# Kernel optimization log

Hardware: AMD Instinct MI355X
Metric: run time of the kernel (lower is better)

Reference implementation:

```python
import jax, jax.numpy as jnp
import numpy as np

DECAY = 0.99
EPS = 1e-05


def setup_inputs() -> dict:
    key = jax.random.key(0)
    k1, k2, k3 = jax.random.split(key, 3)
    B, H, W, D, K = 16, 32, 32, 256, 8192
    x = jax.random.normal(k1, (B, H, W, D), dtype=jnp.float32)
    embed = jax.random.normal(k2, (D, K), dtype=jnp.float32)
    cluster_size = jnp.zeros((K,), dtype=jnp.float32)
    embed_avg = jax.random.normal(k3, (D, K), dtype=jnp.float32)
    return {"x": x, "embed": embed, "cluster_size": cluster_size, "embed_avg": embed_avg}


def reference(x, embed, cluster_size, embed_avg):
    D, K = embed.shape
    flat = x.reshape(-1, D)  # (N, D)
    # squared L2 distances: ||f||^2 - 2 f.e + ||e||^2  -> (N, K)
    dist = (flat * flat).sum(1, keepdims=True) - 2.0 * (flat @ embed) + (embed * embed).sum(0, keepdims=True)
    idx = jnp.argmin(dist, axis=1)  # (N,)
    quantize = jnp.take(embed.T, idx, axis=0).reshape(x.shape)  # (B,H,W,D)
    # EMA codebook statistics (training branch)
    onehot_sum = jnp.zeros((K,), dtype=flat.dtype).at[idx].add(1.0)  # (K,)
    embed_sum = jax.ops.segment_sum(flat, idx, num_segments=K).T  # (D, K)
    new_cluster_size = cluster_size * DECAY + (1.0 - DECAY) * onehot_sum
    new_embed_avg = embed_avg * DECAY + (1.0 - DECAY) * embed_sum
    n = new_cluster_size.sum()
    cs = (new_cluster_size + EPS) / (n + K * EPS) * n
    new_embed = new_embed_avg / cs[None, :]
    latent_loss = jnp.mean((jax.lax.stop_gradient(quantize) - x) ** 2)
    quantize_st = x + jax.lax.stop_gradient(quantize - x)  # straight-through
    return quantize_st, latent_loss, new_embed, new_cluster_size, new_embed_avg
```

## Files before the change

kernel.cpp:

```cpp
#include <hip/hip_runtime.h>

constexpr int NROWS = 16384;
constexpr int D     = 256;
constexpr int K     = 8192;

constexpr float DECAY = 0.99f;
constexpr float OMD   = 0.01f;
constexpr float EPSF  = 1e-5f;

constexpr size_t OUT_Q    = 0;
constexpr size_t OUT_LOSS = (size_t)NROWS * D;
constexpr size_t OUT_NE   = OUT_LOSS + 1;
constexpr size_t OUT_NCS  = OUT_NE + (size_t)D * K;
constexpr size_t OUT_NEA  = OUT_NCS + K;

constexpr size_t WS_KEYS  = 0;
constexpr size_t WS_ENORM = WS_KEYS + (size_t)NROWS * 8;
constexpr size_t WS_XH    = ((WS_ENORM + (size_t)K * 4 + 4095) / 4096) * 4096;
constexpr size_t WS_XL    = WS_XH + (size_t)NROWS * D * 2;
constexpr size_t WS_EHT   = WS_XL + (size_t)NROWS * D * 2;
constexpr size_t WS_ELT   = WS_EHT + (size_t)K * D * 2;

typedef unsigned int u32;
typedef unsigned short u16;
typedef unsigned long long u64;
typedef __attribute__((ext_vector_type(8))) short bf16x8;
typedef __attribute__((ext_vector_type(4))) float f32x4;
typedef __attribute__((ext_vector_type(4))) u32 u32x4;
typedef __attribute__((ext_vector_type(2))) u32 u32x2;

__device__ __forceinline__ u16 f2bf(float f) {
    u32 u = __float_as_uint(f);
    u32 r = (u + 0x7FFFu + ((u >> 16) & 1u)) >> 16;
    return (u16)r;
}
__device__ __forceinline__ float bf2f(u16 h) {
    return __uint_as_float((u32)h << 16);
}

__device__ __forceinline__ void gl_lds16(const void* g, void* l) {
    __builtin_amdgcn_global_load_lds(
        (const __attribute__((address_space(1))) u32*)g,
        (__attribute__((address_space(3))) u32*)l, 16, 0, 0);
}

__global__ void pre_kernel(const float* __restrict__ x,
                           const float* __restrict__ embed,
                           const float* __restrict__ cluster_size,
                           u16* __restrict__ xh, u16* __restrict__ xl,
                           u16* __restrict__ ehT, u16* __restrict__ elT,
                           float* __restrict__ enorm,
                           u64* __restrict__ keys,
                           float* __restrict__ ncs_out,
                           float* __restrict__ loss_out) {
    const int bid = blockIdx.x;
    const int t   = threadIdx.x;

    if (bid >= 176) {
        size_t g = (size_t)(bid - 176) * 256 + t;
        float4 v = *(const float4*)&x[g * 4];
        u16 h0 = f2bf(v.x), h1 = f2bf(v.y), h2 = f2bf(v.z), h3 = f2bf(v.w);
        u16 l0 = f2bf(v.x - bf2f(h0)), l1 = f2bf(v.y - bf2f(h1));
        u16 l2 = f2bf(v.z - bf2f(h2)), l3 = f2bf(v.w - bf2f(h3));
        u32x2 hp, lp;
        hp.x = (u32)h0 | ((u32)h1 << 16); hp.y = (u32)h2 | ((u32)h3 << 16);
        lp.x = (u32)l0 | ((u32)l1 << 16); lp.y = (u32)l2 | ((u32)l3 << 16);
        ((u32x2*)xh)[g] = hp;
        ((u32x2*)xl)[g] = lp;
        return;
    }
    if (bid >= 144) {
        int i = (bid - 144) * 256 + t;
        ncs_out[i] = DECAY * cluster_size[i];
        return;
    }
    if (bid >= 128) {
        int idx = (bid - 128) * 256 + t;
        #pragma unroll
        for (int j = 0; j < 4; ++j) keys[j * 4096 + idx] = ~0ull;
        if (bid == 128 && t == 0) loss_out[0] = 0.f;
        return;
    }

    __shared__ float tile[64][68];
    const int kBase = bid * 64;
    const int dl = t >> 2;
    const int kl = t >> 2;
    const int qq = t & 3;
    float nacc = 0.f;

    for (int dBase = 0; dBase < D; dBase += 64) {
        #pragma unroll
        for (int i = 0; i < 4; ++i) {
            int kk = qq * 16 + i * 4;
            float4 v = *(const float4*)&embed[(size_t)(dBase + dl) * K + kBase + kk];
            tile[dl][kk + 0] = v.x; tile[dl][kk + 1] = v.y;
            tile[dl][kk + 2] = v.z; tile[dl][kk + 3] = v.w;
        }
        __syncthreads();
        u32 hp[8], lp[8];
        float s = 0.f;
        #pragma unroll
        for (int j = 0; j < 16; ++j) {
            float f = tile[qq * 16 + j][kl];
            s = fmaf(f, f, s);
            u16 hb = f2bf(f);
            u16 lb = f2bf(f - bf2f(hb));
            if (j & 1) { hp[j >> 1] |= (u32)hb << 16; lp[j >> 1] |= (u32)lb << 16; }
            else       { hp[j >> 1]  = hb;            lp[j >> 1]  = lb; }
        }
        s += __shfl_down(s, 1);
        s += __shfl_down(s, 2);
        if (qq == 0) nacc += s;

        size_t o = ((size_t)(kBase + kl) * D + dBase + qq * 16) >> 1;
        u32x4 a, b;
        a.x = hp[0]; a.y = hp[1]; a.z = hp[2]; a.w = hp[3];
        b.x = hp[4]; b.y = hp[5]; b.z = hp[6]; b.w = hp[7];
        *(u32x4*)&((u32*)ehT)[o]     = a;
        *(u32x4*)&((u32*)ehT)[o + 4] = b;
        a.x = lp[0]; a.y = lp[1]; a.z = lp[2]; a.w = lp[3];
        b.x = lp[4]; b.y = lp[5]; b.z = lp[6]; b.w = lp[7];
        *(u32x4*)&((u32*)elT)[o]     = a;
        *(u32x4*)&((u32*)elT)[o + 4] = b;
        __syncthreads();
    }
    if (qq == 0) enorm[kBase + kl] = nacc;
}

__global__ __launch_bounds__(512, 2) void dist_argmin_mfma(
        const u16* __restrict__ xh, const u16* __restrict__ xl,
        const u16* __restrict__ ehT, const u16* __restrict__ elT,
        const float* __restrict__ enorm,
        u64* __restrict__ keys) {
    __shared__ u16 lds[2][32768];

    const int tid  = threadIdx.x;
    const int lane = tid & 63;
    const int wave = tid >> 6;
    const int wm   = wave >> 1;
    const int wn   = wave & 1;
    const int r = lane & 15, g = lane >> 4;
    const int rowBase = blockIdx.y * 256;
    const int colBase = blockIdx.x * 256;

    f32x4 acc[4][8];
    #pragma unroll
    for (int i = 0; i < 4; ++i)
        #pragma unroll
        for (int j = 0; j < 8; ++j) acc[i][j] = (f32x4)0.f;

    const int chunk8 = (((tid & 3) ^ ((tid >> 3) & 3)) * 8);
    const int arow   = tid >> 2;
    const size_t a0 = (size_t)(rowBase + arow) * D + chunk8;
    const size_t a1 = (size_t)(rowBase + 128 + arow) * D + chunk8;
    const int bmat   = tid >> 8;
    const int qrow   = (tid & 255) >> 2;
    const int bcol0  = (qrow < 32) ? qrow : (96 + qrow);
    const size_t bq0 = (size_t)(colBase + bcol0) * D + chunk8;
    const u16* bsrc  = bmat ? elT : ehT;

    const int kx = (g ^ ((r >> 1) & 3)) * 8;

    #define ST_XH0(buf, ks) gl_lds16(&xh[a0 + (ks) * 32], &lds[buf][tid * 8])
    #define ST_XH1(buf, ks) gl_lds16(&xh[a1 + (ks) * 32], &lds[buf][4096 + tid * 8])
    #define ST_XL0(buf, ks) gl_lds16(&xl[a0 + (ks) * 32], &lds[buf][8192 + tid * 8])
    #define ST_XL1(buf, ks) gl_lds16(&xl[a1 + (ks) * 32], &lds[buf][12288 + tid * 8])
    #define ST_B(buf, ks, q) \
        gl_lds16(&bsrc[bq0 + (size_t)(q) * 32 * D + (ks) * 32], \
                 &lds[buf][16384 + (q) * 4096 + tid * 8])

    ST_B(0, 0, 0); ST_XH0(0, 0); ST_B(0, 0, 1); ST_XH1(0, 0);
    ST_B(0, 0, 2); ST_XL0(0, 0); ST_B(0, 0, 3); ST_XL1(0, 0);
    ST_B(1, 1, 0); ST_XH0(1, 1); ST_B(1, 1, 1); ST_XH1(1, 1);
    ST_B(1, 1, 2); ST_XL0(1, 1);

    bf16x8 fah[4], fal[4];
    bf16x8 fbhA[2], fblA[2], fbhB[2], fblB[2];

    #define RD_A(Lp)                                                              \
        do { _Pragma("unroll") for (int i_ = 0; i_ < 4; ++i_) {                   \
            fah[i_] = *(const bf16x8*)&(Lp)[((wm * 64 + i_ * 16 + r) * 32) + kx]; \
            fal[i_] = *(const bf16x8*)&(Lp)[8192 + ((wm * 64 + i_ * 16 + r) * 32) + kx]; \
        } } while (0)

    #define RD_B(Lp, p, FH, FL)                                                   \
        do { _Pragma("unroll") for (int jj_ = 0; jj_ < 2; ++jj_) {                \
            const int qr_ = wn * 32 + jj_ * 16 + r;                               \
            (FH)[jj_] = *(const bf16x8*)&(Lp)[16384 + (p) * 4096 + qr_ * 32 + kx];        \
            (FL)[jj_] = *(const bf16x8*)&(Lp)[16384 + (p) * 4096 + 2048 + qr_ * 32 + kx]; \
        } } while (0)

    #define MFMA_PH(p, FH, FL)                                                    \
        do { _Pragma("unroll") for (int i_ = 0; i_ < 4; ++i_) {                   \
            acc[i_][2*(p)]   = __builtin_amdgcn_mfma_f32_16x16x32_bf16(fah[i_], (FH)[0], acc[i_][2*(p)],   0, 0, 0); \
            acc[i_][2*(p)]   = __builtin_amdgcn_mfma_f32_16x16x32_bf16(fah[i_], (FL)[0], acc[i_][2*(p)],   0, 0, 0); \
            acc[i_][2*(p)]   = __builtin_amdgcn_mfma_f32_16x16x32_bf16(fal[i_], (FH)[0], acc[i_][2*(p)],   0, 0, 0); \
            acc[i_][2*(p)+1] = __builtin_amdgcn_mfma_f32_16x16x32_bf16(fah[i_], (FH)[1], acc[i_][2*(p)+1], 0, 0, 0); \
            acc[i_][2*(p)+1] = __builtin_amdgcn_mfma_f32_16x16x32_bf16(fah[i_], (FL)[1], acc[i_][2*(p)+1], 0, 0, 0); \
            acc[i_][2*(p)+1] = __builtin_amdgcn_mfma_f32_16x16x32_bf16(fal[i_], (FH)[1], acc[i_][2*(p)+1], 0, 0, 0); \
        } } while (0)

    #define LGKM4() asm volatile("s_waitcnt lgkmcnt(4)" ::: "memory"); \
                    __builtin_amdgcn_sched_barrier(0)
    #define LGKM0() asm volatile("s_waitcnt lgkmcnt(0)" ::: "memory"); \
                    __builtin_amdgcn_sched_barrier(0)

    #pragma unroll
    for (int ks = 0; ks < 8; ++ks) {
        const int c = ks & 1;
        const u16* L = lds[c];

        if (ks == 7) asm volatile("s_waitcnt vmcnt(0)" ::: "memory");
        else         asm volatile("s_waitcnt vmcnt(6)" ::: "memory");
        __builtin_amdgcn_s_barrier();
        __builtin_amdgcn_sched_barrier(0);

        RD_A(L);
        RD_B(L, 0, fbhA, fblA);
        RD_B(L, 1, fbhB, fblB);
        if (ks <= 6) { ST_B(c ^ 1, ks + 1, 3); ST_XL1(c ^ 1, ks + 1); }
        LGKM4();
        __builtin_amdgcn_s_setprio(1);
        MFMA_PH(0, fbhA, fblA);
        __builtin_amdgcn_s_setprio(0);
        __builtin_amdgcn_s_barrier();
        __builtin_amdgcn_sched_barrier(0);

        RD_B(L, 2, fbhA, fblA);
        if (ks <= 5) { ST_B(c, ks + 2, 0); ST_XH0(c, ks + 2); }
        LGKM4();
        __builtin_amdgcn_s_setprio(1);
        MFMA_PH(1, fbhB, fblB);
        __builtin_amdgcn_s_setprio(0);
        __builtin_amdgcn_s_barrier();
        __builtin_amdgcn_sched_barrier(0);

        RD_B(L, 3, fbhB, fblB);
        if (ks <= 5) { ST_B(c, ks + 2, 1); ST_XH1(c, ks + 2); }
        LGKM4();
        __builtin_amdgcn_s_setprio(1);
        MFMA_PH(2, fbhA, fblA);
        __builtin_amdgcn_s_setprio(0);
        __builtin_amdgcn_s_barrier();
        __builtin_amdgcn_sched_barrier(0);

        if (ks <= 5) { ST_B(c, ks + 2, 2); ST_XL0(c, ks + 2); }
        LGKM0();
        __builtin_amdgcn_s_setprio(1);
        MFMA_PH(3, fbhB, fblB);
        __builtin_amdgcn_s_setprio(0);
        __builtin_amdgcn_s_barrier();
        __builtin_amdgcn_sched_barrier(0);
    }
    #undef MFMA_PH
    #undef RD_A
    #undef RD_B
    #undef LGKM4
    #undef LGKM0
    #undef ST_XH0
    #undef ST_XH1
    #undef ST_XL0
    #undef ST_XL1
    #undef ST_B

    float en[8];
    #pragma unroll
    for (int j = 0; j < 8; ++j) en[j] = enorm[colBase + wn * 128 + j * 16 + r];

    #pragma unroll
    for (int i = 0; i < 4; ++i) {
        #pragma unroll
        for (int p4 = 0; p4 < 4; ++p4) {
            float best = __builtin_inff();
            int bk = 0;
            #pragma unroll
            for (int j = 0; j < 8; ++j) {
                float s = fmaf(-2.f, acc[i][j][p4], en[j]);
                int ccol = colBase + wn * 128 + j * 16 + r;
                if (s < best) { best = s; bk = ccol; }
            }
            u32 u = __float_as_uint(best);
            u ^= (u >> 31) ? 0xFFFFFFFFu : 0x80000000u;
            u64 key = ((u64)u << 32) | (u32)bk;
            #pragma unroll
            for (int m = 1; m < 16; m <<= 1) {
                u64 o = __shfl_xor(key, m);
                key = o < key ? o : key;
            }
            if (r == 0)
                atomicMin(&keys[rowBase + wm * 64 + i * 16 + g * 4 + p4], key);
        }
    }
}

__global__ void postprocess_kernel(const float* __restrict__ x,
                                   const u16* __restrict__ ehT,
                                   const u16* __restrict__ elT,
                                   const u64* __restrict__ keys,
                                   float* __restrict__ q_out,
                                   float* __restrict__ loss_out,
                                   float* __restrict__ acc_t,
                                   float* __restrict__ ncs_out) {
    const int w    = threadIdx.x >> 6;
    const int lane = threadIdx.x & 63;
    const int r    = blockIdx.x * 4 + w;
    const u32 k = (u32)keys[r];

    float4 xv = *(const float4*)&x[(size_t)r * D + lane * 4];
    size_t uo = ((size_t)k * D >> 1) + lane * 2;
    u32x2 hp = *(const u32x2*)&((const u32*)ehT)[uo];
    u32x2 lp = *(const u32x2*)&((const u32*)elT)[uo];
    float q0 = __uint_as_float(hp.x << 16)         + __uint_as_float(lp.x << 16);
    float q1 = __uint_as_float(hp.x & 0xFFFF0000u) + __uint_as_float(lp.x & 0xFFFF0000u);
    float q2 = __uint_as_float(hp.y << 16)         + __uint_as_float(lp.y << 16);
    float q3 = __uint_as_float(hp.y & 0xFFFF0000u) + __uint_as_float(lp.y & 0xFFFF0000u);
    *(float4*)&q_out[(size_t)r * D + lane * 4] = make_float4(q0, q1, q2, q3);

    float* dst = &acc_t[(size_t)k * D + lane * 4];
    atomicAdd(dst + 0, xv.x);
    atomicAdd(dst + 1, xv.y);
    atomicAdd(dst + 2, xv.z);
    atomicAdd(dst + 3, xv.w);
    if (lane == 0) atomicAdd(&ncs_out[k], OMD);

    float d0 = q0 - xv.x, d1 = q1 - xv.y, d2 = q2 - xv.z, d3 = q3 - xv.w;
    float lsum = fmaf(d0, d0, fmaf(d1, d1, fmaf(d2, d2, d3 * d3)));
    #pragma unroll
    for (int off = 32; off > 0; off >>= 1) lsum += __shfl_down(lsum, off);
    __shared__ float wsum[4];
    if (lane == 0) wsum[w] = lsum;
    __syncthreads();
    if (threadIdx.x == 0) {
        float s = wsum[0] + wsum[1] + wsum[2] + wsum[3];
        atomicAdd(loss_out, s * (1.0f / ((float)NROWS * (float)D)));
    }
}

__global__ void ema_finalize_kernel(const float* __restrict__ embed_avg,
                                    const float* __restrict__ acc_t,
                                    const float* __restrict__ ncs_out,
                                    const float* __restrict__ cluster_size,
                                    float* __restrict__ nea_out,
                                    float* __restrict__ ne_out) {
    __shared__ float tile[64][68];
    __shared__ float wsums[4];
    const int kBase = blockIdx.x * 64;
    const int dBase = blockIdx.y * 64;
    const int t = threadIdx.x;

    float cs_part = 0.f;
    #pragma unroll
    for (int j = 0; j < K / 256; ++j) cs_part += cluster_size[j * 256 + t];
    #pragma unroll
    for (int off = 32; off > 0; off >>= 1) cs_part += __shfl_down(cs_part, off);
    if ((t & 63) == 0) wsums[t >> 6] = cs_part;

    {
        const int kl = t >> 2, q = t & 3;
        #pragma unroll
        for (int i = 0; i < 4; ++i) {
            int dd = q * 16 + i * 4;
            float4 v = *(const float4*)&acc_t[(size_t)(kBase + kl) * D + dBase + dd];
            tile[kl][dd + 0] = v.x; tile[kl][dd + 1] = v.y;
            tile[kl][dd + 2] = v.z; tile[kl][dd + 3] = v.w;
        }
    }
    __syncthreads();
    const float cssum = wsums[0] + wsums[1] + wsums[2] + wsums[3];
    const float n = DECAY * cssum + OMD * (float)NROWS;
    const float inv_na = 1.0f / (n + (float)K * EPSF);
    const int dl = t >> 2, q = t & 3;
    #pragma unroll
    for (int i = 0; i < 4; ++i) {
        int kk = q * 16 + i * 4;
        size_t o = (size_t)(dBase + dl) * K + kBase + kk;
        float4 ea = *(const float4*)&embed_avg[o];
        float4 nea, ne;
        #pragma unroll
        for (int c = 0; c < 4; ++c) {
            float v  = DECAY * ((const float*)&ea)[c] + OMD * tile[kk + c][dl];
            float cs = (ncs_out[kBase + kk + c] + EPSF) * inv_na * n;
            ((float*)&nea)[c] = v;
            ((float*)&ne)[c]  = v / cs;
        }
        *(float4*)&nea_out[o] = nea;
        *(float4*)&ne_out[o]  = ne;
    }
}

extern "C" void kernel_launch(void* const* d_in, const int* in_sizes, int n_in,
                              void* d_out, int out_size, void* d_ws, size_t ws_size,
                              hipStream_t stream) {
    (void)in_sizes; (void)n_in; (void)out_size; (void)ws_size;
    const float* x            = (const float*)d_in[0];
    const float* embed        = (const float*)d_in[1];
    const float* cluster_size = (const float*)d_in[2];
    const float* embed_avg    = (const float*)d_in[3];
    float* out = (float*)d_out;

    char* ws = (char*)d_ws;
    u64*   keys  = (u64*)(ws + WS_KEYS);
    float* enorm = (float*)(ws + WS_ENORM);
    u16*   xh    = (u16*)(ws + WS_XH);
    u16*   xl    = (u16*)(ws + WS_XL);
    u16*   ehT   = (u16*)(ws + WS_EHT);
    u16*   elT   = (u16*)(ws + WS_ELT);
    float* acc_t = (float*)(ws + WS_XH);

    float* q_out    = out + OUT_Q;
    float* loss_out = out + OUT_LOSS;
    float* ne_out   = out + OUT_NE;
    float* ncs_out  = out + OUT_NCS;
    float* nea_out  = out + OUT_NEA;

    pre_kernel<<<dim3(176 + NROWS * D / 4 / 256), dim3(256), 0, stream>>>(
        x, embed, cluster_size, xh, xl, ehT, elT, enorm, keys, ncs_out, loss_out);

    dist_argmin_mfma<<<dim3(K / 256, NROWS / 256), dim3(512), 0, stream>>>(
        xh, xl, ehT, elT, enorm, keys);

    hipMemsetAsync(acc_t, 0, (size_t)K * D * 4, stream);
    postprocess_kernel<<<dim3(NROWS / 4), dim3(256), 0, stream>>>(
        x, ehT, elT, keys, q_out, loss_out, acc_t, ncs_out);
    ema_finalize_kernel<<<dim3(K / 64, D / 64), dim3(256), 0, stream>>>(
        embed_avg, acc_t, ncs_out, cluster_size, nea_out, ne_out);
}
```

Measured before the change: 298.5 us.

## Split codebook conversion blocks and precompute cluster-size sum once

```diff
diff --git a/kernel.cpp b/kernel.cpp
--- a/kernel.cpp
+++ b/kernel.cpp
@@ -16,7 +16,8 @@
 
 constexpr size_t WS_KEYS  = 0;
 constexpr size_t WS_ENORM = WS_KEYS + (size_t)NROWS * 8;
-constexpr size_t WS_XH    = ((WS_ENORM + (size_t)K * 4 + 4095) / 4096) * 4096;
+constexpr size_t WS_NSUM  = WS_ENORM + (size_t)K * 4;
+constexpr size_t WS_XH    = ((WS_NSUM + 4096) / 4096) * 4096;
 constexpr size_t WS_XL    = WS_XH + (size_t)NROWS * D * 2;
 constexpr size_t WS_EHT   = WS_XL + (size_t)NROWS * D * 2;
 constexpr size_t WS_ELT   = WS_EHT + (size_t)K * D * 2;
@@ -52,12 +53,13 @@
                            float* __restrict__ enorm,
                            u64* __restrict__ keys,
                            float* __restrict__ ncs_out,
-                           float* __restrict__ loss_out) {
+                           float* __restrict__ loss_out,
+                           float* __restrict__ nsum) {
     const int bid = blockIdx.x;
     const int t   = threadIdx.x;
 
-    if (bid >= 176) {
-        size_t g = (size_t)(bid - 176) * 256 + t;
+    if (bid >= 593) {
+        size_t g = (size_t)(bid - 593) * 256 + t;
         float4 v = *(const float4*)&x[g * 4];
         u16 h0 = f2bf(v.x), h1 = f2bf(v.y), h2 = f2bf(v.z), h3 = f2bf(v.w);
         u16 l0 = f2bf(v.x - bf2f(h0)), l1 = f2bf(v.y - bf2f(h1));
@@ -69,63 +71,81 @@
         ((u32x2*)xl)[g] = lp;
         return;
     }
-    if (bid >= 144) {
-        int i = (bid - 144) * 256 + t;
+    if (bid == 592) {
+        __shared__ float ws4[4];
+        float v = 0.f;
+        #pragma unroll
+        for (int j = 0; j < K / 256; ++j) v += cluster_size[j * 256 + t];
+        #pragma unroll
+        for (int off = 32; off > 0; off >>= 1) v += __shfl_down(v, off);
+        if ((t & 63) == 0) ws4[t >> 6] = v;
+        __syncthreads();
+        if (t == 0) {
+            nsum[0] = ws4[0] + ws4[1] + ws4[2] + ws4[3];
+            loss_out[0] = 0.f;
+        }
+        return;
+    }
+    if (bid >= 560) {
+        int i = (bid - 560) * 256 + t;
         ncs_out[i] = DECAY * cluster_size[i];
         return;
     }
-    if (bid >= 128) {
-        int idx = (bid - 128) * 256 + t;
+    if (bid >= 544) {
+        int idx = (bid - 544) * 256 + t;
         #pragma unroll
         for (int j = 0; j < 4; ++j) keys[j * 4096 + idx] = ~0ull;
-        if (bid == 128 && t == 0) loss_out[0] = 0.f;
         return;
     }
+    if (bid >= 512) {
+        int k = (bid - 512) * 256 + t;
+        float a0 = 0.f, a1 = 0.f, a2 = 0.f, a3 = 0.f;
+        for (int d = 0; d < D; d += 4) {
+            float e0 = embed[(size_t)(d + 0) * K + k];
+            float e1 = embed[(size_t)(d + 1) * K + k];
+            float e2 = embed[(size_t)(d + 2) * K + k];
+            float e3 = embed[(size_t)(d + 3) * K + k];
+            a0 = fmaf(e0, e0, a0); a1 = fmaf(e1, e1, a1);
+            a2 = fmaf(e2, e2, a2); a3 = fmaf(e3, e3, a3);
+        }
+        enorm[k] = (a0 + a1) + (a2 + a3);
+        return;
+    }
 
     __shared__ float tile[64][68];
-    const int kBase = bid * 64;
-    const int dl = t >> 2;
-    const int kl = t >> 2;
-    const int qq = t & 3;
-    float nacc = 0.f;
-
-    for (int dBase = 0; dBase < D; dBase += 64) {
+    const int kBase = (bid >> 2) * 64;
+    const int dBase = (bid & 3) * 64;
+    {
+        const int dl = t >> 2, q = t & 3;
         #pragma unroll
         for (int i = 0; i < 4; ++i) {
-            int kk = qq * 16 + i * 4;
+            int kk = q * 16 + i * 4;
             float4 v = *(const float4*)&embed[(size_t)(dBase + dl) * K + kBase + kk];
             tile[dl][kk + 0] = v.x; tile[dl][kk + 1] = v.y;
             tile[dl][kk + 2] = v.z; tile[dl][kk + 3] = v.w;
         }
-        __syncthreads();
-        u32 hp[8], lp[8];
-        float s = 0.f;
-        #pragma unroll
-        for (int j = 0; j < 16; ++j) {
-            float f = tile[qq * 16 + j][kl];
-            s = fmaf(f, f, s);
-            u16 hb = f2bf(f);
-            u16 lb = f2bf(f - bf2f(hb));
-            if (j & 1) { hp[j >> 1] |= (u32)hb << 16; lp[j >> 1] |= (u32)lb << 16; }
-            else       { hp[j >> 1]  = hb;            lp[j >> 1]  = lb; }
-        }
-        s += __shfl_down(s, 1);
-        s += __shfl_down(s, 2);
-        if (qq == 0) nacc += s;
-
-        size_t o = ((size_t)(kBase + kl) * D + dBase + qq * 16) >> 1;
-        u32x4 a, b;
-        a.x = hp[0]; a.y = hp[1]; a.z = hp[2]; a.w = hp[3];
-        b.x = hp[4]; b.y = hp[5]; b.z = hp[6]; b.w = hp[7];
-        *(u32x4*)&((u32*)ehT)[o]     = a;
-        *(u32x4*)&((u32*)ehT)[o + 4] = b;
-        a.x = lp[0]; a.y = lp[1]; a.z = lp[2]; a.w = lp[3];
-        b.x = lp[4]; b.y = lp[5]; b.z = lp[6]; b.w = lp[7];
-        *(u32x4*)&((u32*)elT)[o]     = a;
-        *(u32x4*)&((u32*)elT)[o + 4] = b;
-        __syncthreads();
-    }
-    if (qq == 0) enorm[kBase + kl] = nacc;
+    }
+    __syncthreads();
+    const int kl = t >> 2, q = t & 3;
+    u32 hp[8], lp[8];
+    #pragma unroll
+    for (int j = 0; j < 16; ++j) {
+        float f = tile[q * 16 + j][kl];
+        u16 hb = f2bf(f);
+        u16 lb = f2bf(f - bf2f(hb));
+        if (j & 1) { hp[j >> 1] |= (u32)hb << 16; lp[j >> 1] |= (u32)lb << 16; }
+        else       { hp[j >> 1]  = hb;            lp[j >> 1]  = lb; }
+    }
+    size_t o = ((size_t)(kBase + kl) * D + dBase + q * 16) >> 1;
+    u32x4 a, b;
+    a.x = hp[0]; a.y = hp[1]; a.z = hp[2]; a.w = hp[3];
+    b.x = hp[4]; b.y = hp[5]; b.z = hp[6]; b.w = hp[7];
+    *(u32x4*)&((u32*)ehT)[o]     = a;
+    *(u32x4*)&((u32*)ehT)[o + 4] = b;
+    a.x = lp[0]; a.y = lp[1]; a.z = lp[2]; a.w = lp[3];
+    b.x = lp[4]; b.y = lp[5]; b.z = lp[6]; b.w = lp[7];
+    *(u32x4*)&((u32*)elT)[o]     = a;
+    *(u32x4*)&((u32*)elT)[o + 4] = b;
 }
 
 __global__ __launch_bounds__(512, 2) void dist_argmin_mfma(
@@ -340,22 +360,13 @@
 __global__ void ema_finalize_kernel(const float* __restrict__ embed_avg,
                                     const float* __restrict__ acc_t,
                                     const float* __restrict__ ncs_out,
-                                    const float* __restrict__ cluster_size,
+                                    const float* __restrict__ nsum,
                                     float* __restrict__ nea_out,
                                     float* __restrict__ ne_out) {
     __shared__ float tile[64][68];
-    __shared__ float wsums[4];
     const int kBase = blockIdx.x * 64;
     const int dBase = blockIdx.y * 64;
     const int t = threadIdx.x;
-
-    float cs_part = 0.f;
-    #pragma unroll
-    for (int j = 0; j < K / 256; ++j) cs_part += cluster_size[j * 256 + t];
-    #pragma unroll
-    for (int off = 32; off > 0; off >>= 1) cs_part += __shfl_down(cs_part, off);
-    if ((t & 63) == 0) wsums[t >> 6] = cs_part;
-
     {
         const int kl = t >> 2, q = t & 3;
         #pragma unroll
@@ -367,8 +378,7 @@
         }
     }
     __syncthreads();
-    const float cssum = wsums[0] + wsums[1] + wsums[2] + wsums[3];
-    const float n = DECAY * cssum + OMD * (float)NROWS;
+    const float n = DECAY * nsum[0] + OMD * (float)NROWS;
     const float inv_na = 1.0f / (n + (float)K * EPSF);
     const int dl = t >> 2, q = t & 3;
     #pragma unroll
@@ -402,6 +412,7 @@
     char* ws = (char*)d_ws;
     u64*   keys  = (u64*)(ws + WS_KEYS);
     float* enorm = (float*)(ws + WS_ENORM);
+    float* nsum  = (float*)(ws + WS_NSUM);
     u16*   xh    = (u16*)(ws + WS_XH);
     u16*   xl    = (u16*)(ws + WS_XL);
     u16*   ehT   = (u16*)(ws + WS_EHT);
@@ -414,8 +425,9 @@
     float* ncs_out  = out + OUT_NCS;
     float* nea_out  = out + OUT_NEA;
 
-    pre_kernel<<<dim3(176 + NROWS * D / 4 / 256), dim3(256), 0, stream>>>(
-        x, embed, cluster_size, xh, xl, ehT, elT, enorm, keys, ncs_out, loss_out);
+    pre_kernel<<<dim3(593 + NROWS * D / 4 / 256), dim3(256), 0, stream>>>(
+        x, embed, cluster_size, xh, xl, ehT, elT, enorm, keys, ncs_out,
+        loss_out, nsum);
 
     dist_argmin_mfma<<<dim3(K / 256, NROWS / 256), dim3(512), 0, stream>>>(
         xh, xl, ehT, elT, enorm, keys);
@@ -424,5 +436,5 @@
     postprocess_kernel<<<dim3(NROWS / 4), dim3(256), 0, stream>>>(
         x, ehT, elT, keys, q_out, loss_out, acc_t, ncs_out);
     ema_finalize_kernel<<<dim3(K / 64, D / 64), dim3(256), 0, stream>>>(
-        embed_avg, acc_t, ncs_out, cluster_size, nea_out, ne_out);
-}
+        embed_avg, acc_t, ncs_out, nsum, nea_out, ne_out);
+}
```

Measured after the change: 339.8 us. 1.14x slower.
